# Performance work log

Hardware: AMD Instinct MI355X
Metric: run time of the kernel (lower is better)

Reference implementation:

```python
import jax, jax.numpy as jnp
import numpy as np

WIDTH = 4096
NUM_HEADS = 8
BLOCK_W = WIDTH // NUM_HEADS


def _block_diag_linear(x, w, b):
    # x: [n, width] -> [n, h, bw]; w: [h, bw, bw]; b: [h, bw]
    n = x.shape[0]
    xh = x.reshape(n, NUM_HEADS, BLOCK_W)
    y = jnp.einsum('nhi,hij->nhj', xh, w) + b
    return y.reshape(n, WIDTH)


def setup_inputs() -> dict:
    key = jax.random.key(0)
    ks = jax.random.split(key, 7)
    n = 8192
    x = jax.random.normal(ks[0], (n, WIDTH), dtype=jnp.float32)
    s = jnp.sort(jax.random.randint(ks[1], (n,), 0, 8, dtype=jnp.int32))
    # a_param init: uniform on ring radii [0.9, 0.999], softplus-inverse transform
    eps = 1e-8
    u = jax.random.uniform(ks[2], (WIDTH,), minval=0.9**2 + eps, maxval=0.999**2 + eps)
    t = 0.5 * jnp.log(u)
    a_param = jnp.log(jnp.exp(-t) - 1.0).astype(jnp.float32)
    std = 1.0 / np.sqrt(BLOCK_W)
    ig_w = std * jax.random.normal(ks[3], (NUM_HEADS, BLOCK_W, BLOCK_W), dtype=jnp.float32)
    ig_b = jnp.zeros((NUM_HEADS, BLOCK_W), dtype=jnp.float32)
    ag_w = std * jax.random.normal(ks[4], (NUM_HEADS, BLOCK_W, BLOCK_W), dtype=jnp.float32)
    ag_b = jnp.zeros((NUM_HEADS, BLOCK_W), dtype=jnp.float32)
    return {'x': x, 's': s, 'a_param': a_param, 'ig_w': ig_w, 'ig_b': ig_b,
            'ag_w': ag_w, 'ag_b': ag_b}


def reference(x, s, a_param, ig_w, ig_b, ag_w, ag_b):
    n, k = x.shape
    # reset mask: True at position 0 and wherever segment id changes
    reset = jnp.concatenate([jnp.ones((1,), dtype=bool), s[1:] != s[:-1]])
    gate_x = jax.nn.sigmoid(_block_diag_linear(x, ig_w, ig_b))
    gate_a = jax.nn.sigmoid(_block_diag_linear(x, ag_w, ag_b))
    log_a = -8.0 * gate_a * jax.nn.softplus(a_param)  # [n, k]
    a = jnp.exp(log_a)
    a_square = jnp.exp(2.0 * log_a)
    multiplier = jnp.sqrt(1.0 - a_square)
    multiplier = jnp.where(reset[:, None], 1.0, multiplier)
    normalized_x = x * gate_x * multiplier
    # linear recurrence h[t] = a[t] * h[t-1] + normalized_x[t] via parallel scan
    def combine(e1, e2):
        a1, b1 = e1
        a2, b2 = e2
        return (a1 * a2, a2 * b1 + b2)
    _, out = jax.lax.associative_scan(combine, (a, normalized_x), axis=0)
    return out
```

## Files before the change

### kernel.cpp

```cpp
#include <hip/hip_runtime.h>
#include <hip/hip_bf16.h>
#include <stdint.h>

#define WIDTH 4096
#define NROWS 8192
#define NHEADS 8
#define BW 512
#define CS 128
#define NCHUNK (NROWS/CS)

typedef short bf16x8 __attribute__((ext_vector_type(8)));
typedef float f32x4 __attribute__((ext_vector_type(4)));

__device__ __forceinline__ uint32_t rne_bf16(float f) {
  uint32_t u = __float_as_uint(f);
  return (u + 0x7fffu + ((u >> 16) & 1u)) >> 16;
}
__device__ __forceinline__ uint32_t pack2(float lo, float hi) {
  return rne_bf16(lo) | (rne_bf16(hi) << 16);
}
__device__ __forceinline__ float bf16_to_f32(uint32_t bits) {
  return __uint_as_float(bits << 16);
}
__device__ __forceinline__ uint32_t cvtpk(float a, float b) {
  uint32_t r;
  asm("v_cvt_pk_bf16_f32 %0, %1, %2" : "=v"(r) : "v"(a), "v"(b));
  return r;
}

__device__ __forceinline__ void gload_lds16(const void* g, void* l) {
  __builtin_amdgcn_global_load_lds(
      (const __attribute__((address_space(1))) void*)g,
      (__attribute__((address_space(3))) void*)l, 16, 0, 0);
}

__global__ void prep_xbf16(const float* __restrict__ x, uint16_t* __restrict__ xb) {
  size_t i = ((size_t)blockIdx.x * 256 + threadIdx.x) * 8;
  float4 f0 = *reinterpret_cast<const float4*>(x + i);
  float4 f1 = *reinterpret_cast<const float4*>(x + i + 4);
  uint4 v;
  v.x = pack2(f0.x, f0.y); v.y = pack2(f0.z, f0.w);
  v.z = pack2(f1.x, f1.y); v.w = pack2(f1.z, f1.w);
  *reinterpret_cast<uint4*>(xb + i) = v;
}

__global__ void prep_weights(const float* __restrict__ ig_w,
                             const float* __restrict__ ag_w,
                             uint16_t* __restrict__ wt) {
  __shared__ float tile[32][33];
  int j0 = blockIdx.x * 32;
  int i0 = blockIdx.y * 32;
  int m  = blockIdx.z;
  const float* src = ((m >> 3) ? ag_w : ig_w) + (size_t)(m & 7) * BW * BW;
  int tx = threadIdx.x & 31, ty = threadIdx.x >> 5;
  #pragma unroll
  for (int k = 0; k < 4; k++) {
    int i = i0 + ty + 8 * k;
    tile[ty + 8 * k][tx] = src[(size_t)i * BW + (j0 + tx)];
  }
  __syncthreads();
  #pragma unroll
  for (int k = 0; k < 4; k++) {
    int j = j0 + ty + 8 * k;
    wt[((size_t)m * BW + j) * BW + (i0 + tx)] = (uint16_t)rne_bf16(tile[tx][ty + 8 * k]);
  }
}

__global__ void prep_misc(const float* __restrict__ a_param, float* __restrict__ cvec) {
  int i = blockIdx.x * 256 + threadIdx.x;
  if (i < WIDTH) {
    float x = a_param[i];
    float sp = (x > 15.f) ? x : log1pf(expf(x));
    cvec[i] = 8.f * sp;
  }
}

#define BM 128
#define BN 64
#define BK 64

__global__ __launch_bounds__(256, 4)
void gates_gemm(const uint16_t* __restrict__ xb,
                const int* __restrict__ s,
                const uint16_t* __restrict__ wt,
                const float* __restrict__ ig_b,
                const float* __restrict__ ag_b,
                const float* __restrict__ cvec,
                uint32_t* __restrict__ lanx,
                float* __restrict__ cA,
                float* __restrict__ cB) {
  __shared__ __align__(16) unsigned char dsm[32768];
  __shared__ unsigned char resetm[BM];

  const int b = blockIdx.x;
  const int orig = (b & 7) * 512 + (b >> 3);
  const int h  = orig >> 9;
  const int rem = orig & 511;
  const int mt = rem >> 3;
  const int nt = rem & 7;
  const int m0 = mt * BM;
  const int j0 = nt * BN;

  const int tid = threadIdx.x;
  const int lane = tid & 63;
  const int w = tid >> 6;
  const int wr = w >> 1;
  const int wc = w & 1;
  const int lrow = lane & 15;
  const int lkg  = lane >> 4;

  if (tid < BM) {
    int n = m0 + tid;
    resetm[tid] = (n == 0) || (s[n] != s[n - 1]);
  }

  const char* xb_src[4];
  #pragma unroll
  for (int i = 0; i < 4; i++) {
    int o = i * 4096 + tid * 16;
    int row = o >> 7;
    int c = (o & 127) ^ ((row & 7) << 4);
    xb_src[i] = (const char*)xb + (size_t)(m0 + row) * (WIDTH * 2) + h * (BW * 2) + c;
  }
  const char* w_src[4];
  #pragma unroll
  for (int i = 0; i < 4; i++) {
    int o = i * 4096 + tid * 16;
    int g = o >> 13;
    int jl = (o >> 7) & 63;
    int c = (o & 127) ^ ((jl & 7) << 4);
    w_src[i] = (const char*)wt + ((size_t)((g * 8 + h) * BW + (j0 + jl))) * (BW * 2) + c;
  }

  f32x4 acc[2][4][2];
  #pragma unroll
  for (int g = 0; g < 2; g++)
    #pragma unroll
    for (int mf = 0; mf < 4; mf++)
      #pragma unroll
      for (int nf = 0; nf < 2; nf++)
        acc[g][mf][nf] = (f32x4){0.f, 0.f, 0.f, 0.f};

  for (int kt = 0; kt < 8; kt++) {
    const int p = (nt + 1 + kt) & 7;
    __syncthreads();
    #pragma unroll
    for (int i = 0; i < 4; i++)
      gload_lds16(xb_src[i] + p * 128, dsm + i * 4096 + tid * 16);
    #pragma unroll
    for (int i = 0; i < 4; i++)
      gload_lds16(w_src[i] + p * 128, dsm + 16384 + i * 4096 + tid * 16);
    __syncthreads();
    #pragma unroll
    for (int ks = 0; ks < 2; ks++) {
      bf16x8 af[4];
      #pragma unroll
      for (int mf = 0; mf < 4; mf++) {
        int row = wr * 64 + 16 * mf + lrow;
        uint32_t addr = (uint32_t)((row << 7) + ks * 64 + lkg * 16);
        addr ^= (uint32_t)((row & 7) << 4);
        af[mf] = *reinterpret_cast<const bf16x8*>(dsm + addr);
      }
      #pragma unroll
      for (int g = 0; g < 2; g++) {
        #pragma unroll
        for (int nf = 0; nf < 2; nf++) {
          int j = wc * 32 + 16 * nf + lrow;
          uint32_t addr = (uint32_t)(16384 + (g << 13) + (j << 7) + ks * 64 + lkg * 16);
          addr ^= (uint32_t)((j & 7) << 4);
          bf16x8 bfr = *reinterpret_cast<const bf16x8*>(dsm + addr);
          #pragma unroll
          for (int mf = 0; mf < 4; mf++) {
            acc[g][mf][nf] = __builtin_amdgcn_mfma_f32_16x16x32_bf16(
                af[mf], bfr, acc[g][mf][nf], 0, 0, 0);
          }
        }
      }
    }
  }
  __syncthreads();

  float* smf = (float*)(dsm + 16384);

  const int jl0 = wc * 32 + lrow;
  float igb[2], agb[2], cv2[2];
  #pragma unroll
  for (int nf = 0; nf < 2; nf++) {
    int jj = h * BW + j0 + jl0 + 16 * nf;
    igb[nf] = ig_b[jj]; agb[nf] = ag_b[jj]; cv2[nf] = cvec[jj];
  }

  float segA[2][4], segB[2][4];
  #pragma unroll
  for (int mf = 0; mf < 4; mf++) {
    float A[2] = {1.f, 1.f}, B[2] = {0.f, 0.f};
    int rbase = wr * 64 + 16 * mf + 4 * lkg;
    #pragma unroll
    for (int r = 0; r < 4; r++) {
      int row = rbase + r;
      int n = m0 + row;
      bool rs = resetm[row] != 0;
      uint32_t xswz = (uint32_t)((row & 7) << 4);
      #pragma unroll
      for (int nf = 0; nf < 2; nf++) {
        int jl = jl0 + 16 * nf;
        size_t o = (size_t)n * WIDTH + h * BW + j0 + jl;
        float yig = acc[0][mf][nf][r] + igb[nf];
        float yag = acc[1][mf][nf][r] + agb[nf];
        float gx = __builtin_amdgcn_rcpf(1.f + __expf(-yig));
        float ga = __builtin_amdgcn_rcpf(1.f + __expf(-yag));
        float la = -ga * cv2[nf];
        float la_r = bf16_to_f32(cvtpk(la, la) & 0xffffu);
        float a = __expf(la_r);
        float mult = rs ? 1.f
                     : __builtin_amdgcn_sqrtf(fmaxf(1.f - a * a, 0.f));
        uint32_t xaddr = ((uint32_t)((row << 7) + jl * 2)) ^ xswz;
        float xv = bf16_to_f32(*reinterpret_cast<const uint16_t*>(dsm + xaddr));
        float nx = xv * gx * mult;
        uint32_t word = cvtpk(la_r, nx);
        float nx_r = __uint_as_float(word & 0xffff0000u);
        lanx[o] = word;
        A[nf] *= a;
        B[nf] = fmaf(a, B[nf], nx_r);
      }
    }
    segA[0][mf] = A[0]; segB[0][mf] = B[0];
    segA[1][mf] = A[1]; segB[1][mf] = B[1];
  }
  #pragma unroll
  for (int nf = 0; nf < 2; nf++) {
    #pragma unroll
    for (int mf = 0; mf < 4; mf++) {
      float A = segA[nf][mf], B = segB[nf][mf];
      #pragma unroll
      for (int d = 16; d <= 32; d <<= 1) {
        float pA = __shfl_xor(A, d, 64);
        float pB = __shfl_xor(B, d, 64);
        bool up = (lane & d) != 0;
        B = up ? fmaf(A, pB, B) : fmaf(pA, B, pB);
        A *= pA;
      }
      segA[nf][mf] = A; segB[nf][mf] = B;
    }
    float colA = segA[nf][0], colB = segB[nf][0];
    #pragma unroll
    for (int mf = 1; mf < 4; mf++) {
      colB = fmaf(segA[nf][mf], colB, segB[nf][mf]);
      colA *= segA[nf][mf];
    }
    if (lkg == 0) {
      int clocal = wc * 32 + 16 * nf + lrow;
      smf[wr * 64 + clocal] = colA;
      smf[128 + wr * 64 + clocal] = colB;
    }
  }
  __syncthreads();
  if (tid < BN) {
    float A0 = smf[tid],       B0 = smf[128 + tid];
    float A1 = smf[64 + tid],  B1 = smf[192 + tid];
    float Af = A0 * A1;
    float Bf = fmaf(A1, B0, B1);
    int jj = h * BW + j0 + tid;
    cA[mt * WIDTH + jj] = Af;
    cB[mt * WIDTH + jj] = Bf;
  }
}

__global__ void scan_prefix(const float* __restrict__ cA, const float* __restrict__ cB,
                            float* __restrict__ prefix) {
  int c = blockIdx.x * 256 + threadIdx.x;
  float hcur = 0.f;
  for (int i0 = 0; i0 < NCHUNK; i0 += 8) {
    float av[8], bv[8];
    #pragma unroll
    for (int e = 0; e < 8; e++) { av[e] = cA[(i0 + e) * WIDTH + c]; bv[e] = cB[(i0 + e) * WIDTH + c]; }
    #pragma unroll
    for (int e = 0; e < 8; e++) { prefix[(i0 + e) * WIDTH + c] = hcur; hcur = av[e] * hcur + bv[e]; }
  }
}

__global__ void scan_apply(const uint32_t* __restrict__ lanx,
                           const float* __restrict__ prefix,
                           float* __restrict__ out) {
  int chunk = blockIdx.x;
  int c0 = (blockIdx.y * 256 + threadIdx.x) * 4;
  size_t base = (size_t)chunk * CS * WIDTH + c0;
  float h[4];
  #pragma unroll
  for (int q = 0; q < 4; q++) h[q] = prefix[chunk * WIDTH + c0 + q];
  for (int rb = 0; rb < CS; rb += 4) {
    uint4 v[4];
    #pragma unroll
    for (int e = 0; e < 4; e++)
      v[e] = *reinterpret_cast<const uint4*>(lanx + base + (size_t)(rb + e) * WIDTH);
    #pragma unroll
    for (int e = 0; e < 4; e++) {
      float4 ov;
      h[0] = fmaf(__expf(bf16_to_f32(v[e].x & 0xffffu)), h[0], bf16_to_f32(v[e].x >> 16)); ov.x = h[0];
      h[1] = fmaf(__expf(bf16_to_f32(v[e].y & 0xffffu)), h[1], bf16_to_f32(v[e].y >> 16)); ov.y = h[1];
      h[2] = fmaf(__expf(bf16_to_f32(v[e].z & 0xffffu)), h[2], bf16_to_f32(v[e].z >> 16)); ov.z = h[2];
      h[3] = fmaf(__expf(bf16_to_f32(v[e].w & 0xffffu)), h[3], bf16_to_f32(v[e].w >> 16)); ov.w = h[3];
      *reinterpret_cast<float4*>(out + base + (size_t)(rb + e) * WIDTH) = ov;
    }
  }
}

extern "C" void kernel_launch(void* const* d_in, const int* in_sizes, int n_in,
                              void* d_out, int out_size, void* d_ws, size_t ws_size,
                              hipStream_t stream) {
  const float* x       = (const float*)d_in[0];
  const int*   s       = (const int*)d_in[1];
  const float* a_param = (const float*)d_in[2];
  const float* ig_w    = (const float*)d_in[3];
  const float* ig_b    = (const float*)d_in[4];
  const float* ag_w    = (const float*)d_in[5];
  const float* ag_b    = (const float*)d_in[6];
  float* out = (float*)d_out;
  char* ws = (char*)d_ws;

  uint32_t* lanx   = (uint32_t*)ws;
  uint16_t* wt     = (uint16_t*)(ws + 134217728);
  uint16_t* xb     = (uint16_t*)(ws + 142606336);
  float*    cvec   = (float*)(ws + 209715200);
  float*    cA     = (float*)(ws + 209731584);
  float*    cB     = (float*)(ws + 210780160);
  float*    prefix = (float*)(ws + 211828736);

  prep_xbf16<<<dim3(16384), 256, 0, stream>>>(x, xb);
  prep_weights<<<dim3(16, 16, 16), 256, 0, stream>>>(ig_w, ag_w, wt);
  prep_misc<<<dim3(16), 256, 0, stream>>>(a_param, cvec);
  gates_gemm<<<dim3(4096), 256, 0, stream>>>(xb, s, wt, ig_b, ag_b, cvec,
                                             lanx, cA, cB);
  scan_prefix<<<dim3(16), 256, 0, stream>>>(cA, cB, prefix);
  scan_apply<<<dim3(NCHUNK, 4), 256, 0, stream>>>(lanx, prefix, out);
}
```

Measured before the change: 213.4 us.

## Double-buffer GEMM K loop, fuse prep kernels, fold scan prefix into apply

```diff
diff --git a/kernel.cpp b/kernel.cpp
--- a/kernel.cpp
+++ b/kernel.cpp
@@ -8,6 +8,7 @@
 #define BW 512
 #define CS 128
 #define NCHUNK (NROWS/CS)
+#define LOG2E 1.4426950408889634f
 
 typedef short bf16x8 __attribute__((ext_vector_type(8)));
 typedef float f32x4 __attribute__((ext_vector_type(4)));
@@ -15,9 +16,6 @@
 __device__ __forceinline__ uint32_t rne_bf16(float f) {
   uint32_t u = __float_as_uint(f);
   return (u + 0x7fffu + ((u >> 16) & 1u)) >> 16;
-}
-__device__ __forceinline__ uint32_t pack2(float lo, float hi) {
-  return rne_bf16(lo) | (rne_bf16(hi) << 16);
 }
 __device__ __forceinline__ float bf16_to_f32(uint32_t bits) {
   return __uint_as_float(bits << 16);
@@ -34,50 +32,55 @@
       (__attribute__((address_space(3))) void*)l, 16, 0, 0);
 }
 
-__global__ void prep_xbf16(const float* __restrict__ x, uint16_t* __restrict__ xb) {
-  size_t i = ((size_t)blockIdx.x * 256 + threadIdx.x) * 8;
-  float4 f0 = *reinterpret_cast<const float4*>(x + i);
-  float4 f1 = *reinterpret_cast<const float4*>(x + i + 4);
-  uint4 v;
-  v.x = pack2(f0.x, f0.y); v.y = pack2(f0.z, f0.w);
-  v.z = pack2(f1.x, f1.y); v.w = pack2(f1.z, f1.w);
-  *reinterpret_cast<uint4*>(xb + i) = v;
-}
-
-__global__ void prep_weights(const float* __restrict__ ig_w,
-                             const float* __restrict__ ag_w,
-                             uint16_t* __restrict__ wt) {
+__global__ void prep_all(const float* __restrict__ x, uint16_t* __restrict__ xb,
+                         const float* __restrict__ ig_w, const float* __restrict__ ag_w,
+                         uint16_t* __restrict__ wt,
+                         const float* __restrict__ a_param, float* __restrict__ cvec2) {
   __shared__ float tile[32][33];
-  int j0 = blockIdx.x * 32;
-  int i0 = blockIdx.y * 32;
-  int m  = blockIdx.z;
-  const float* src = ((m >> 3) ? ag_w : ig_w) + (size_t)(m & 7) * BW * BW;
-  int tx = threadIdx.x & 31, ty = threadIdx.x >> 5;
-  #pragma unroll
-  for (int k = 0; k < 4; k++) {
-    int i = i0 + ty + 8 * k;
-    tile[ty + 8 * k][tx] = src[(size_t)i * BW + (j0 + tx)];
-  }
-  __syncthreads();
-  #pragma unroll
-  for (int k = 0; k < 4; k++) {
-    int j = j0 + ty + 8 * k;
-    wt[((size_t)m * BW + j) * BW + (i0 + tx)] = (uint16_t)rne_bf16(tile[tx][ty + 8 * k]);
-  }
-}
-
-__global__ void prep_misc(const float* __restrict__ a_param, float* __restrict__ cvec) {
-  int i = blockIdx.x * 256 + threadIdx.x;
-  if (i < WIDTH) {
-    float x = a_param[i];
-    float sp = (x > 15.f) ? x : log1pf(expf(x));
-    cvec[i] = 8.f * sp;
+  const int b = blockIdx.x;
+  const int tid = threadIdx.x;
+  if (b < 4096) {
+    int m  = b >> 8;
+    int j0 = ((b >> 4) & 15) * 32;
+    int i0 = (b & 15) * 32;
+    const float* src = ((m >> 3) ? ag_w : ig_w) + (size_t)(m & 7) * BW * BW;
+    int tx = tid & 31, ty = tid >> 5;
+    #pragma unroll
+    for (int k = 0; k < 4; k++) {
+      int i = i0 + ty + 8 * k;
+      tile[ty + 8 * k][tx] = src[(size_t)i * BW + (j0 + tx)] * LOG2E;
+    }
+    __syncthreads();
+    #pragma unroll
+    for (int k = 0; k < 4; k++) {
+      int j = j0 + ty + 8 * k;
+      wt[((size_t)m * BW + j) * BW + (i0 + tx)] = (uint16_t)rne_bf16(tile[tx][ty + 8 * k]);
+    }
+  } else if (b < 6144) {
+    int bb = b - 4096;
+    #pragma unroll
+    for (int it = 0; it < 8; it++) {
+      size_t i = (((size_t)it * 2048 + bb) * 256 + tid) * 8;
+      float4 f0 = *reinterpret_cast<const float4*>(x + i);
+      float4 f1 = *reinterpret_cast<const float4*>(x + i + 4);
+      uint4 v;
+      v.x = cvtpk(f0.x, f0.y); v.y = cvtpk(f0.z, f0.w);
+      v.z = cvtpk(f1.x, f1.y); v.w = cvtpk(f1.z, f1.w);
+      *reinterpret_cast<uint4*>(xb + i) = v;
+    }
+  } else {
+    int i = (b - 6144) * 256 + tid;
+    if (i < WIDTH) {
+      float v = a_param[i];
+      float sp = (v > 15.f) ? v : log1pf(expf(v));
+      cvec2[i] = 8.f * sp * LOG2E;
+    }
   }
 }
 
 #define BM 128
 #define BN 64
-#define BK 64
+#define BK 32
 
 __global__ __launch_bounds__(256, 4)
 void gates_gemm(const uint16_t* __restrict__ xb,
@@ -85,7 +88,7 @@
                 const uint16_t* __restrict__ wt,
                 const float* __restrict__ ig_b,
                 const float* __restrict__ ag_b,
-                const float* __restrict__ cvec,
+                const float* __restrict__ cvec2,
                 uint32_t* __restrict__ lanx,
                 float* __restrict__ cA,
                 float* __restrict__ cB) {
@@ -114,22 +117,24 @@
     resetm[tid] = (n == 0) || (s[n] != s[n - 1]);
   }
 
-  const char* xb_src[4];
-  #pragma unroll
-  for (int i = 0; i < 4; i++) {
+  const char* xb_src[2];
+  #pragma unroll
+  for (int i = 0; i < 2; i++) {
     int o = i * 4096 + tid * 16;
-    int row = o >> 7;
-    int c = (o & 127) ^ ((row & 7) << 4);
-    xb_src[i] = (const char*)xb + (size_t)(m0 + row) * (WIDTH * 2) + h * (BW * 2) + c;
-  }
-  const char* w_src[4];
-  #pragma unroll
-  for (int i = 0; i < 4; i++) {
+    int row = o >> 6;
+    int cc = o & 63;
+    int cbyte = ((((cc >> 4) ^ ((row >> 1) & 3)) << 4)) | (cc & 15);
+    xb_src[i] = (const char*)xb + (size_t)(m0 + row) * (WIDTH * 2) + h * (BW * 2) + cbyte;
+  }
+  const char* w_src[2];
+  #pragma unroll
+  for (int i = 0; i < 2; i++) {
     int o = i * 4096 + tid * 16;
-    int g = o >> 13;
-    int jl = (o >> 7) & 63;
-    int c = (o & 127) ^ ((jl & 7) << 4);
-    w_src[i] = (const char*)wt + ((size_t)((g * 8 + h) * BW + (j0 + jl))) * (BW * 2) + c;
+    int g = o >> 12;
+    int jl = (o >> 6) & 63;
+    int cc = o & 63;
+    int cbyte = ((((cc >> 4) ^ ((jl >> 1) & 3)) << 4)) | (cc & 15);
+    w_src[i] = (const char*)wt + ((size_t)((g * 8 + h) * BW + (j0 + jl))) * (BW * 2) + cbyte;
   }
 
   f32x4 acc[2][4][2];
@@ -141,53 +146,65 @@
       for (int nf = 0; nf < 2; nf++)
         acc[g][mf][nf] = (f32x4){0.f, 0.f, 0.f, 0.f};
 
-  for (int kt = 0; kt < 8; kt++) {
-    const int p = (nt + 1 + kt) & 7;
-    __syncthreads();
-    #pragma unroll
-    for (int i = 0; i < 4; i++)
-      gload_lds16(xb_src[i] + p * 128, dsm + i * 4096 + tid * 16);
-    #pragma unroll
-    for (int i = 0; i < 4; i++)
-      gload_lds16(w_src[i] + p * 128, dsm + 16384 + i * 4096 + tid * 16);
-    __syncthreads();
-    #pragma unroll
-    for (int ks = 0; ks < 2; ks++) {
-      bf16x8 af[4];
-      #pragma unroll
-      for (int mf = 0; mf < 4; mf++) {
-        int row = wr * 64 + 16 * mf + lrow;
-        uint32_t addr = (uint32_t)((row << 7) + ks * 64 + lkg * 16);
-        addr ^= (uint32_t)((row & 7) << 4);
-        af[mf] = *reinterpret_cast<const bf16x8*>(dsm + addr);
-      }
-      #pragma unroll
-      for (int g = 0; g < 2; g++) {
+  {
+    const int p0 = (2 * nt + 2) & 15;
+    #pragma unroll
+    for (int i = 0; i < 2; i++)
+      gload_lds16(xb_src[i] + p0 * 64, dsm + i * 4096 + tid * 16);
+    #pragma unroll
+    for (int i = 0; i < 2; i++)
+      gload_lds16(w_src[i] + p0 * 64, dsm + 8192 + i * 4096 + tid * 16);
+  }
+  __syncthreads();
+
+  for (int st = 0; st < 16; st++) {
+    const uint32_t bufb = (uint32_t)(st & 1) << 14;
+    if (st < 15) {
+      const uint32_t nb = bufb ^ 16384u;
+      const int p = (2 * nt + 3 + st) & 15;
+      #pragma unroll
+      for (int i = 0; i < 2; i++)
+        gload_lds16(xb_src[i] + p * 64, dsm + nb + i * 4096 + tid * 16);
+      #pragma unroll
+      for (int i = 0; i < 2; i++)
+        gload_lds16(w_src[i] + p * 64, dsm + nb + 8192 + i * 4096 + tid * 16);
+    }
+    bf16x8 af[4];
+    #pragma unroll
+    for (int mf = 0; mf < 4; mf++) {
+      int row = wr * 64 + 16 * mf + lrow;
+      uint32_t addr = bufb + (uint32_t)(row << 6)
+                    + (uint32_t)((lkg << 4) ^ (((row >> 1) & 3) << 4));
+      af[mf] = *reinterpret_cast<const bf16x8*>(dsm + addr);
+    }
+    __builtin_amdgcn_s_setprio(1);
+    #pragma unroll
+    for (int g = 0; g < 2; g++) {
+      #pragma unroll
+      for (int nf = 0; nf < 2; nf++) {
+        int j = wc * 32 + 16 * nf + lrow;
+        uint32_t addr = bufb + 8192u + (uint32_t)(g << 12) + (uint32_t)(j << 6)
+                      + (uint32_t)((lkg << 4) ^ (((j >> 1) & 3) << 4));
+        bf16x8 bfr = *reinterpret_cast<const bf16x8*>(dsm + addr);
         #pragma unroll
-        for (int nf = 0; nf < 2; nf++) {
-          int j = wc * 32 + 16 * nf + lrow;
-          uint32_t addr = (uint32_t)(16384 + (g << 13) + (j << 7) + ks * 64 + lkg * 16);
-          addr ^= (uint32_t)((j & 7) << 4);
-          bf16x8 bfr = *reinterpret_cast<const bf16x8*>(dsm + addr);
-          #pragma unroll
-          for (int mf = 0; mf < 4; mf++) {
-            acc[g][mf][nf] = __builtin_amdgcn_mfma_f32_16x16x32_bf16(
-                af[mf], bfr, acc[g][mf][nf], 0, 0, 0);
-          }
+        for (int mf = 0; mf < 4; mf++) {
+          acc[g][mf][nf] = __builtin_amdgcn_mfma_f32_16x16x32_bf16(
+              af[mf], bfr, acc[g][mf][nf], 0, 0, 0);
         }
       }
     }
-  }
-  __syncthreads();
-
-  float* smf = (float*)(dsm + 16384);
+    __builtin_amdgcn_s_setprio(0);
+    __syncthreads();
+  }
+
+  float* smf = (float*)(dsm + 8192);
 
   const int jl0 = wc * 32 + lrow;
   float igb[2], agb[2], cv2[2];
   #pragma unroll
   for (int nf = 0; nf < 2; nf++) {
     int jj = h * BW + j0 + jl0 + 16 * nf;
-    igb[nf] = ig_b[jj]; agb[nf] = ag_b[jj]; cv2[nf] = cvec[jj];
+    igb[nf] = ig_b[jj] * LOG2E; agb[nf] = ag_b[jj] * LOG2E; cv2[nf] = cvec2[jj];
   }
 
   float segA[2][4], segB[2][4];
@@ -200,21 +217,23 @@
       int row = rbase + r;
       int n = m0 + row;
       bool rs = resetm[row] != 0;
-      uint32_t xswz = (uint32_t)((row & 7) << 4);
+      uint32_t xsw = (uint32_t)(((row >> 1) & 3) << 4);
       #pragma unroll
       for (int nf = 0; nf < 2; nf++) {
         int jl = jl0 + 16 * nf;
         size_t o = (size_t)n * WIDTH + h * BW + j0 + jl;
         float yig = acc[0][mf][nf][r] + igb[nf];
         float yag = acc[1][mf][nf][r] + agb[nf];
-        float gx = __builtin_amdgcn_rcpf(1.f + __expf(-yig));
-        float ga = __builtin_amdgcn_rcpf(1.f + __expf(-yag));
-        float la = -ga * cv2[nf];
-        float la_r = bf16_to_f32(cvtpk(la, la) & 0xffffu);
-        float a = __expf(la_r);
+        float gx = __builtin_amdgcn_rcpf(1.f + exp2f(-yig));
+        float ga = __builtin_amdgcn_rcpf(1.f + exp2f(-yag));
+        float la2 = -ga * cv2[nf];
+        float la_r = bf16_to_f32(cvtpk(la2, la2) & 0xffffu);
+        float a = exp2f(la_r);
         float mult = rs ? 1.f
                      : __builtin_amdgcn_sqrtf(fmaxf(1.f - a * a, 0.f));
-        uint32_t xaddr = ((uint32_t)((row << 7) + jl * 2)) ^ xswz;
+        int cb = (jl & 31) * 2;
+        uint32_t xaddr = ((jl >> 5) ? 16384u : 0u) + (uint32_t)(row << 6)
+                       + (uint32_t)(((uint32_t)(cb >> 4) << 4) ^ xsw) + (uint32_t)(cb & 15);
         float xv = bf16_to_f32(*reinterpret_cast<const uint16_t*>(dsm + xaddr));
         float nx = xv * gx * mult;
         uint32_t word = cvtpk(la_r, nx);
@@ -266,28 +285,22 @@
   }
 }
 
-__global__ void scan_prefix(const float* __restrict__ cA, const float* __restrict__ cB,
-                            float* __restrict__ prefix) {
-  int c = blockIdx.x * 256 + threadIdx.x;
-  float hcur = 0.f;
-  for (int i0 = 0; i0 < NCHUNK; i0 += 8) {
-    float av[8], bv[8];
-    #pragma unroll
-    for (int e = 0; e < 8; e++) { av[e] = cA[(i0 + e) * WIDTH + c]; bv[e] = cB[(i0 + e) * WIDTH + c]; }
-    #pragma unroll
-    for (int e = 0; e < 8; e++) { prefix[(i0 + e) * WIDTH + c] = hcur; hcur = av[e] * hcur + bv[e]; }
-  }
-}
-
 __global__ void scan_apply(const uint32_t* __restrict__ lanx,
-                           const float* __restrict__ prefix,
+                           const float* __restrict__ cA,
+                           const float* __restrict__ cB,
                            float* __restrict__ out) {
   int chunk = blockIdx.x;
   int c0 = (blockIdx.y * 256 + threadIdx.x) * 4;
   size_t base = (size_t)chunk * CS * WIDTH + c0;
-  float h[4];
-  #pragma unroll
-  for (int q = 0; q < 4; q++) h[q] = prefix[chunk * WIDTH + c0 + q];
+  float h[4] = {0.f, 0.f, 0.f, 0.f};
+  for (int i = 0; i < chunk; i++) {
+    float4 av = *reinterpret_cast<const float4*>(cA + i * WIDTH + c0);
+    float4 bv = *reinterpret_cast<const float4*>(cB + i * WIDTH + c0);
+    h[0] = fmaf(av.x, h[0], bv.x);
+    h[1] = fmaf(av.y, h[1], bv.y);
+    h[2] = fmaf(av.z, h[2], bv.z);
+    h[3] = fmaf(av.w, h[3], bv.w);
+  }
   for (int rb = 0; rb < CS; rb += 4) {
     uint4 v[4];
     #pragma unroll
@@ -296,10 +309,10 @@
     #pragma unroll
     for (int e = 0; e < 4; e++) {
       float4 ov;
-      h[0] = fmaf(__expf(bf16_to_f32(v[e].x & 0xffffu)), h[0], bf16_to_f32(v[e].x >> 16)); ov.x = h[0];
-      h[1] = fmaf(__expf(bf16_to_f32(v[e].y & 0xffffu)), h[1], bf16_to_f32(v[e].y >> 16)); ov.y = h[1];
-      h[2] = fmaf(__expf(bf16_to_f32(v[e].z & 0xffffu)), h[2], bf16_to_f32(v[e].z >> 16)); ov.z = h[2];
-      h[3] = fmaf(__expf(bf16_to_f32(v[e].w & 0xffffu)), h[3], bf16_to_f32(v[e].w >> 16)); ov.w = h[3];
+      h[0] = fmaf(exp2f(bf16_to_f32(v[e].x & 0xffffu)), h[0], bf16_to_f32(v[e].x >> 16)); ov.x = h[0];
+      h[1] = fmaf(exp2f(bf16_to_f32(v[e].y & 0xffffu)), h[1], bf16_to_f32(v[e].y >> 16)); ov.y = h[1];
+      h[2] = fmaf(exp2f(bf16_to_f32(v[e].z & 0xffffu)), h[2], bf16_to_f32(v[e].z >> 16)); ov.z = h[2];
+      h[3] = fmaf(exp2f(bf16_to_f32(v[e].w & 0xffffu)), h[3], bf16_to_f32(v[e].w >> 16)); ov.w = h[3];
       *reinterpret_cast<float4*>(out + base + (size_t)(rb + e) * WIDTH) = ov;
     }
   }
@@ -321,16 +334,12 @@
   uint32_t* lanx   = (uint32_t*)ws;
   uint16_t* wt     = (uint16_t*)(ws + 134217728);
   uint16_t* xb     = (uint16_t*)(ws + 142606336);
-  float*    cvec   = (float*)(ws + 209715200);
+  float*    cvec2  = (float*)(ws + 209715200);
   float*    cA     = (float*)(ws + 209731584);
   float*    cB     = (float*)(ws + 210780160);
-  float*    prefix = (float*)(ws + 211828736);
-
-  prep_xbf16<<<dim3(16384), 256, 0, stream>>>(x, xb);
-  prep_weights<<<dim3(16, 16, 16), 256, 0, stream>>>(ig_w, ag_w, wt);
-  prep_misc<<<dim3(16), 256, 0, stream>>>(a_param, cvec);
-  gates_gemm<<<dim3(4096), 256, 0, stream>>>(xb, s, wt, ig_b, ag_b, cvec,
+
+  prep_all<<<dim3(6160), 256, 0, stream>>>(x, xb, ig_w, ag_w, wt, a_param, cvec2);
+  gates_gemm<<<dim3(4096), 256, 0, stream>>>(xb, s, wt, ig_b, ag_b, cvec2,
                                              lanx, cA, cB);
-  scan_prefix<<<dim3(16), 256, 0, stream>>>(cA, cB, prefix);
-  scan_apply<<<dim3(NCHUNK, 4), 256, 0, stream>>>(lanx, prefix, out);
-}
+  scan_apply<<<dim3(NCHUNK, 4), 256, 0, stream>>>(lanx, cA, cB, out);
+}
```

Measured after the change: 224.8 us. 5.3% more time.
